# Kernel tuning notes

Hardware: AMD Instinct MI355X
Metric: run time of the kernel (lower is better)

## Reference

```python
import jax, jax.numpy as jnp
import numpy as np


def _patch_indices():
    # 36 positions (6x6 grid), each gathering a 3x3 window of 6-channel squares
    # from the flattened 385-vector: index = x*48 + y*6 + c
    idx = []
    for i in range(36):
        x, y = i // 6, i % 6
        rows = []
        for ox in range(3):
            for oy in range(3):
                base = (x + ox) * 48 + (y + oy) * 6
                rows.extend(range(base, base + 6))
        idx.append(rows)
    return jnp.asarray(np.array(idx, dtype=np.int32))  # [36, 54]


_IDX = _patch_indices()


def _crelu(v):
    return jnp.clip(v, -1.0, 1.0)


def setup_inputs() -> dict:
    key = jax.random.key(0)
    ks = jax.random.split(key, 13)
    B = 131072
    inp = jax.random.normal(ks[0], (B, 385), dtype=jnp.float32)
    s = 0.2  # small init scale
    # sight stack: 54 -> 8 -> 8 -> 1  (stored as [in, out])
    W1 = jax.random.normal(ks[1], (54, 8), jnp.float32) * s
    b1 = jax.random.normal(ks[2], (8,), jnp.float32) * s
    W2 = jax.random.normal(ks[3], (8, 8), jnp.float32) * s
    b2 = jax.random.normal(ks[4], (8,), jnp.float32) * s
    W3 = jax.random.normal(ks[5], (8, 1), jnp.float32) * s
    b3 = jax.random.normal(ks[6], (1,), jnp.float32) * s
    # evaluation stack: 37 -> 16 -> 16 -> 1
    E1 = jax.random.normal(ks[7], (37, 16), jnp.float32) * s
    c1 = jax.random.normal(ks[8], (16,), jnp.float32) * s
    E2 = jax.random.normal(ks[9], (16, 16), jnp.float32) * s
    c2 = jax.random.normal(ks[10], (16,), jnp.float32) * s
    E3 = jax.random.normal(ks[11], (16, 1), jnp.float32) * s
    c3 = jax.random.normal(ks[12], (1,), jnp.float32) * s
    return {"inp": inp, "W1": W1, "b1": b1, "W2": W2, "b2": b2,
            "W3": W3, "b3": b3, "E1": E1, "c1": c1, "E2": E2, "c2": c2,
            "E3": E3, "c3": c3}


def reference(inp, W1, b1, W2, b2, W3, b3, E1, c1, E2, c2, E3, c3):
    # inp: [B, 385]
    patches = inp[:, _IDX]                       # [B, 36, 54] windowed gather
    h = _crelu(jnp.einsum('bpf,fo->bpo', patches, W1) + b1)   # [B, 36, 8]
    h = _crelu(jnp.einsum('bpf,fo->bpo', h, W2) + b2)         # [B, 36, 8]
    v = _crelu(jnp.einsum('bpf,fo->bpo', h, W3) + b3)[..., 0]  # [B, 36]
    vision = jnp.concatenate([v, inp[:, 384:385]], axis=1)    # [B, 37]
    g = _crelu(vision @ E1 + c1)                 # [B, 16]
    g = _crelu(g @ E2 + c2)                      # [B, 16]
    out = _crelu(g @ E3 + c3)                    # [B, 1]
    return out
```

## Files before the change

### kernel.cpp

```cpp
#include <hip/hip_runtime.h>

typedef __attribute__((ext_vector_type(8))) short short8;
typedef __attribute__((ext_vector_type(4))) float float4v;

__device__ __forceinline__ float crelu(float v) {
    return fminf(1.0f, fmaxf(-1.0f, v));
}
__device__ __forceinline__ uint f2bf_u(float v) {
    uint u = __float_as_uint(v);
    u += 0x7fffu + ((u >> 16) & 1u);
    return u >> 16;
}
__device__ __forceinline__ ushort f2bf(float v) { return (ushort)f2bf_u(v); }
__device__ __forceinline__ float bf2f_lo(uint u) { return __uint_as_float(u << 16); }
__device__ __forceinline__ float bf2f_hi(uint u) { return __uint_as_float(u & 0xffff0000u); }

#define ROW 385
#define BT  16

#define SLAB_BYTES 6656
#define E1T_OFF 1024
#define E2T_OFF 3584

__global__ __launch_bounds__(256, 6)
void lila_wave(const float* __restrict__ inp,
               const float* __restrict__ W1, const float* __restrict__ b1,
               const float* __restrict__ W2, const float* __restrict__ b2,
               const float* __restrict__ W3, const float* __restrict__ b3,
               const float* __restrict__ E1, const float* __restrict__ c1,
               const float* __restrict__ E2, const float* __restrict__ c2,
               const float* __restrict__ E3, const float* __restrict__ c3,
               float* __restrict__ out)
{
    __shared__ __align__(16) char slab_all[4 * SLAB_BYTES];

    const int tid  = threadIdx.x;
    const int lane = tid & 63;
    const int wv   = tid >> 6;
    const int quad = lane >> 4;
    const int nn   = lane & 15;
    const int m0   = quad * 8;

    char*   slab  = slab_all + wv * SLAB_BYTES;
    ushort* board = (ushort*)slab;
    ushort* hbuf  = (ushort*)(slab + 4352);
    float*  vis   = (float*)slab;
    float*  g1    = (float*)(slab + 640);
    float*  e1t   = (float*)(slab + E1T_OFF);
    ushort* e2t   = (ushort*)(slab + E2T_OFF);

    const long long b0w = (long long)blockIdx.x * BT + wv * 4;

    short8 bfr[3];
    #pragma unroll
    for (int r = 0; r < 3; ++r) {
        #pragma unroll
        for (int j = 0; j < 8; ++j) {
            int k = m0 + j, oy = k >> 3, c = k & 7;
            float w = (oy < 3 && c < 6 && nn < 8)
                    ? W1[(r * 18 + oy * 6 + c) * 8 + nn] : 0.0f;
            bfr[r][j] = (short)f2bf(w);
        }
    }
    const float bias1 = (nn < 8) ? b1[nn] : 0.0f;

    const int r   = lane >> 4;
    const int c16 = lane & 15;
    const float* gr = inp + (b0w + r) * ROW;

    if (c16 < 4) {
        uint4 z = {0u, 0u, 0u, 0u};
        *(uint4*)(board + r * 544 + 512 + c16 * 8) = z;
    }
    #pragma unroll
    for (int u = 0; u < 4; ++u) {
        int cell = c16 + 16 * u;
        int g = cell * 6;
        float2 p0 = *(const float2*)(gr + g);
        float2 p1 = *(const float2*)(gr + g + 2);
        float2 p2 = *(const float2*)(gr + g + 4);
        uint4 pk;
        pk.x = f2bf_u(p0.x) | (f2bf_u(p0.y) << 16);
        pk.y = f2bf_u(p1.x) | (f2bf_u(p1.y) << 16);
        pk.z = f2bf_u(p2.x) | (f2bf_u(p2.y) << 16);
        pk.w = 0u;
        *(uint4*)(board + r * 544 + cell * 8) = pk;
    }
    const float cen = gr[384];

    asm volatile("" ::: "memory");

    #pragma unroll 3
    for (int t = 0; t < 9; ++t) {
        int ltask = t * 16 + nn;
        uint lb = (uint)ltask / 36u;
        uint p  = (uint)ltask - 36u * lb;
        uint x  = p / 6u;
        uint y  = p - 6u * x;
        const ushort* base = board + lb * 544 + x * 64 + 8 * y + m0;
        union { uint4 u; short8 s; } a0, a1, a2;
        a0.u = *(const uint4*)(base);
        a1.u = *(const uint4*)(base + 64);
        a2.u = *(const uint4*)(base + 128);
        float4v acc = { bias1, bias1, bias1, bias1 };
        acc = __builtin_amdgcn_mfma_f32_16x16x32_bf16(a0.s, bfr[0], acc, 0, 0, 0);
        acc = __builtin_amdgcn_mfma_f32_16x16x32_bf16(a1.s, bfr[1], acc, 0, 0, 0);
        acc = __builtin_amdgcn_mfma_f32_16x16x32_bf16(a2.s, bfr[2], acc, 0, 0, 0);
        if (nn < 8) {
            #pragma unroll
            for (int i = 0; i < 4; ++i)
                hbuf[(t * 16 + quad * 4 + i) * 8 + nn] = f2bf(crelu(acc[i]));
        }
    }

    asm volatile("" ::: "memory");

    {
        float e1g[10];
        #pragma unroll
        for (int k = 0; k < 9; ++k) e1g[k] = E1[lane + 64 * k];
        if (lane < 16) e1g[9] = E1[lane + 576];
        float e2g[4];
        #pragma unroll
        for (int k = 0; k < 4; ++k) e2g[k] = E2[lane + 64 * k];

        #pragma unroll
        for (int k = 0; k < 9; ++k) e1t[nn * 40 + r + 4 * k] = e1g[k];
        if (lane < 16) e1t[nn * 40 + 36] = e1g[9];
        #pragma unroll
        for (int k = 0; k < 4; ++k) e2t[nn * 16 + r + 4 * k] = f2bf(e2g[k]);
    }
    const float c1v = c1[nn];
    const float c2v = c2[nn];
    const float e3v = E3[nn];

    asm volatile("" ::: "memory");

    #pragma unroll 1
    for (int it = 0; it < 3; ++it) {
        int task = lane + it * 64;
        if (task < 144) {
            uint lb = (uint)task / 36u;
            uint p  = (uint)task - 36u * lb;
            uint4 hv = *(const uint4*)(hbuf + task * 8);
            float h[8];
            h[0] = bf2f_lo(hv.x); h[1] = bf2f_hi(hv.x);
            h[2] = bf2f_lo(hv.y); h[3] = bf2f_hi(hv.y);
            h[4] = bf2f_lo(hv.z); h[5] = bf2f_hi(hv.z);
            h[6] = bf2f_lo(hv.w); h[7] = bf2f_hi(hv.w);

            float a2[8];
            #pragma unroll
            for (int o = 0; o < 8; ++o) a2[o] = b2[o];
            #pragma unroll
            for (int i = 0; i < 8; ++i) {
                #pragma unroll
                for (int o = 0; o < 8; ++o)
                    a2[o] = fmaf(h[i], W2[i * 8 + o], a2[o]);
            }
            float v = b3[0];
            #pragma unroll
            for (int i = 0; i < 8; ++i) v = fmaf(crelu(a2[i]), W3[i], v);
            vis[lb * 40 + p] = crelu(v);
        }
    }

    asm volatile("" ::: "memory");

    {
        const int o = nn;
        float a = c1v;
        #pragma unroll
        for (int fi = 0; fi < 9; ++fi) {
            float4 vv = *(const float4*)(vis + r * 40 + fi * 4);
            float4 ev = *(const float4*)(e1t + o * 40 + fi * 4);
            a = fmaf(vv.x, ev.x, a);
            a = fmaf(vv.y, ev.y, a);
            a = fmaf(vv.z, ev.z, a);
            a = fmaf(vv.w, ev.w, a);
        }
        a = fmaf(cen, e1t[o * 40 + 36], a);
        g1[r * 20 + o] = crelu(a);

        asm volatile("" ::: "memory");

        uint4 e2a = *(const uint4*)(e2t + o * 16);
        uint4 e2b = *(const uint4*)(e2t + o * 16 + 8);
        float a2 = c2v;
        #pragma unroll
        for (int fi = 0; fi < 4; ++fi) {
            float4 gv = *(const float4*)(g1 + r * 20 + fi * 4);
            uint w01 = (fi < 2) ? (fi == 0 ? e2a.x : e2a.z) : (fi == 2 ? e2b.x : e2b.z);
            uint w23 = (fi < 2) ? (fi == 0 ? e2a.y : e2a.w) : (fi == 2 ? e2b.y : e2b.w);
            a2 = fmaf(gv.x, bf2f_lo(w01), a2);
            a2 = fmaf(gv.y, bf2f_hi(w01), a2);
            a2 = fmaf(gv.z, bf2f_lo(w23), a2);
            a2 = fmaf(gv.w, bf2f_hi(w23), a2);
        }
        float tv = crelu(a2) * e3v;
        tv += __shfl_xor(tv, 1);
        tv += __shfl_xor(tv, 2);
        tv += __shfl_xor(tv, 4);
        tv += __shfl_xor(tv, 8);
        if (o == 0) out[b0w + r] = crelu(tv + c3[0]);
    }
}

extern "C" void kernel_launch(void* const* d_in, const int* in_sizes, int n_in,
                              void* d_out, int out_size, void* d_ws, size_t ws_size,
                              hipStream_t stream)
{
    const float* inp = (const float*)d_in[0];
    const float* W1  = (const float*)d_in[1];
    const float* b1  = (const float*)d_in[2];
    const float* W2  = (const float*)d_in[3];
    const float* b2  = (const float*)d_in[4];
    const float* W3  = (const float*)d_in[5];
    const float* b3  = (const float*)d_in[6];
    const float* E1  = (const float*)d_in[7];
    const float* c1  = (const float*)d_in[8];
    const float* E2  = (const float*)d_in[9];
    const float* c2  = (const float*)d_in[10];
    const float* E3  = (const float*)d_in[11];
    const float* c3  = (const float*)d_in[12];
    float* out = (float*)d_out;

    int B = in_sizes[0] / ROW;
    int grid = B / BT;
    lila_wave<<<grid, 256, 0, stream>>>(inp, W1, b1, W2, b2, W3, b3,
                                        E1, c1, E2, c2, E3, c3, out);
}
```

Measured before the change: 295.8 us.

## Move second sight layer to MFMA with split bf16 weights and packed conversions

Replaces the scalar per-task 8x8 layer-2 FMA loop and the W3 dot product with bf16 MFMA tiles. Each wave processes two task sets side by side in one 16x16 tile. W2 is split into high and low bf16 parts so the result stays close to fp32 weight precision, and the W3 reduction is done with lane shuffles. It also uses the hardware v_cvt_pk_bf16_f32 instruction for packing, widens the input loads to float4 plus float2, and pads the E1 transpose stride to 44 to reduce LDS bank conflicts. The aim is to cut VALU work in the patch stage, at the cost of running the h activations through bf16 MFMA and some wasted tile rows.

```diff
diff --git a/kernel.cpp b/kernel.cpp
--- a/kernel.cpp
+++ b/kernel.cpp
@@ -14,13 +14,19 @@
 __device__ __forceinline__ ushort f2bf(float v) { return (ushort)f2bf_u(v); }
 __device__ __forceinline__ float bf2f_lo(uint u) { return __uint_as_float(u << 16); }
 __device__ __forceinline__ float bf2f_hi(uint u) { return __uint_as_float(u & 0xffff0000u); }
+__device__ __forceinline__ uint cvt_pk_bf16(float a, float b) {
+    uint r;
+    asm("v_cvt_pk_bf16_f32 %0, %1, %2" : "=v"(r) : "v"(a), "v"(b));
+    return r;
+}
 
 #define ROW 385
 #define BT  16
 
 #define SLAB_BYTES 6656
-#define E1T_OFF 1024
-#define E2T_OFF 3584
+#define E1T_OFF 960
+#define E2T_OFF 3776
+#define E1T_LD  44
 
 __global__ __launch_bounds__(256, 6)
 void lila_wave(const float* __restrict__ inp,
@@ -76,13 +82,12 @@
     for (int u = 0; u < 4; ++u) {
         int cell = c16 + 16 * u;
         int g = cell * 6;
-        float2 p0 = *(const float2*)(gr + g);
-        float2 p1 = *(const float2*)(gr + g + 2);
-        float2 p2 = *(const float2*)(gr + g + 4);
+        float4 q0 = *(const float4*)(gr + g);
+        float2 q1 = *(const float2*)(gr + g + 4);
         uint4 pk;
-        pk.x = f2bf_u(p0.x) | (f2bf_u(p0.y) << 16);
-        pk.y = f2bf_u(p1.x) | (f2bf_u(p1.y) << 16);
-        pk.z = f2bf_u(p2.x) | (f2bf_u(p2.y) << 16);
+        pk.x = cvt_pk_bf16(q0.x, q0.y);
+        pk.y = cvt_pk_bf16(q0.z, q0.w);
+        pk.z = cvt_pk_bf16(q1.x, q1.y);
         pk.w = 0u;
         *(uint4*)(board + r * 544 + cell * 8) = pk;
     }
@@ -107,9 +112,13 @@
         acc = __builtin_amdgcn_mfma_f32_16x16x32_bf16(a1.s, bfr[1], acc, 0, 0, 0);
         acc = __builtin_amdgcn_mfma_f32_16x16x32_bf16(a2.s, bfr[2], acc, 0, 0, 0);
         if (nn < 8) {
-            #pragma unroll
-            for (int i = 0; i < 4; ++i)
-                hbuf[(t * 16 + quad * 4 + i) * 8 + nn] = f2bf(crelu(acc[i]));
+            uint w01 = cvt_pk_bf16(crelu(acc[0]), crelu(acc[1]));
+            uint w23 = cvt_pk_bf16(crelu(acc[2]), crelu(acc[3]));
+            ushort* hb = hbuf + (t * 16 + quad * 4) * 8 + nn;
+            hb[0]  = (ushort)w01;
+            hb[8]  = (ushort)(w01 >> 16);
+            hb[16] = (ushort)w23;
+            hb[24] = (ushort)(w23 >> 16);
         }
     }
 
@@ -125,8 +134,8 @@
         for (int k = 0; k < 4; ++k) e2g[k] = E2[lane + 64 * k];
 
         #pragma unroll
-        for (int k = 0; k < 9; ++k) e1t[nn * 40 + r + 4 * k] = e1g[k];
-        if (lane < 16) e1t[nn * 40 + 36] = e1g[9];
+        for (int k = 0; k < 9; ++k) e1t[nn * E1T_LD + r + 4 * k] = e1g[k];
+        if (lane < 16) e1t[nn * E1T_LD + 36] = e1g[9];
         #pragma unroll
         for (int k = 0; k < 4; ++k) e2t[nn * 16 + r + 4 * k] = f2bf(e2g[k]);
     }
@@ -136,32 +145,52 @@
 
     asm volatile("" ::: "memory");
 
-    #pragma unroll 1
-    for (int it = 0; it < 3; ++it) {
-        int task = lane + it * 64;
-        if (task < 144) {
-            uint lb = (uint)task / 36u;
-            uint p  = (uint)task - 36u * lb;
-            uint4 hv = *(const uint4*)(hbuf + task * 8);
-            float h[8];
-            h[0] = bf2f_lo(hv.x); h[1] = bf2f_hi(hv.x);
-            h[2] = bf2f_lo(hv.y); h[3] = bf2f_hi(hv.y);
-            h[4] = bf2f_lo(hv.z); h[5] = bf2f_hi(hv.z);
-            h[6] = bf2f_lo(hv.w); h[7] = bf2f_hi(hv.w);
-
-            float a2[8];
+    {
+        short8 w2fh, w2fl;
+        const int colq = nn - quad * 8;
+        #pragma unroll
+        for (int j = 0; j < 8; ++j) {
+            float w = (quad < 2 && colq >= 0 && colq < 8) ? W2[j * 8 + colq] : 0.0f;
+            uint hb = f2bf_u(w);
+            float wr = w - __uint_as_float(hb << 16);
+            w2fh[j] = (short)hb;
+            w2fl[j] = (short)f2bf(wr);
+        }
+        const float b2v = b2[nn & 7];
+        const float w3v = W3[nn & 7];
+        const float b3v = b3[0];
+
+        #pragma unroll
+        for (int t = 0; t < 5; ++t) {
+            union { uint4 u; short8 s; } av;
+            av.u.x = 0u; av.u.y = 0u; av.u.z = 0u; av.u.w = 0u;
+            int tsk = t * 16 + nn + (quad ? 80 : 0);
+            if (quad < 2 && (t < 4 || quad == 0))
+                av.u = *(const uint4*)(hbuf + tsk * 8);
+            float4v acc = { b2v, b2v, b2v, b2v };
+            acc = __builtin_amdgcn_mfma_f32_16x16x32_bf16(av.s, w2fh, acc, 0, 0, 0);
+            acc = __builtin_amdgcn_mfma_f32_16x16x32_bf16(av.s, w2fl, acc, 0, 0, 0);
+            float vsum[4];
             #pragma unroll
-            for (int o = 0; o < 8; ++o) a2[o] = b2[o];
-            #pragma unroll
-            for (int i = 0; i < 8; ++i) {
-                #pragma unroll
-                for (int o = 0; o < 8; ++o)
-                    a2[o] = fmaf(h[i], W2[i * 8 + o], a2[o]);
+            for (int i = 0; i < 4; ++i) {
+                float vv = crelu(acc[i]) * w3v;
+                vv += __shfl_xor(vv, 1);
+                vv += __shfl_xor(vv, 2);
+                vv += __shfl_xor(vv, 4);
+                vsum[i] = vv;
             }
-            float v = b3[0];
-            #pragma unroll
-            for (int i = 0; i < 8; ++i) v = fmaf(crelu(a2[i]), W3[i], v);
-            vis[lb * 40 + p] = crelu(v);
+            const bool isA = (nn == 0);
+            if ((nn & 7) == 0 && (isA || t < 4)) {
+                int task = (isA ? 0 : 80) + t * 16 + quad * 4;
+                uint lb = (uint)task / 36u;
+                uint p  = (uint)task - 36u * lb;
+                float4 o4;
+                o4.x = crelu(vsum[0] + b3v);
+                o4.y = crelu(vsum[1] + b3v);
+                o4.z = crelu(vsum[2] + b3v);
+                o4.w = crelu(vsum[3] + b3v);
+                *(float4*)(vis + lb * 40 + p) = o4;
+            }
         }
     }
 
@@ -173,13 +202,13 @@
         #pragma unroll
         for (int fi = 0; fi < 9; ++fi) {
             float4 vv = *(const float4*)(vis + r * 40 + fi * 4);
-            float4 ev = *(const float4*)(e1t + o * 40 + fi * 4);
+            float4 ev = *(const float4*)(e1t + o * E1T_LD + fi * 4);
             a = fmaf(vv.x, ev.x, a);
             a = fmaf(vv.y, ev.y, a);
             a = fmaf(vv.z, ev.z, a);
             a = fmaf(vv.w, ev.w, a);
         }
-        a = fmaf(cen, e1t[o * 40 + 36], a);
+        a = fmaf(cen, e1t[o * E1T_LD + 36], a);
         g1[r * 20 + o] = crelu(a);
 
         asm volatile("" ::: "memory");
```

Result: no change. 293.9 us (-0.6%).
